# Kernel tuning notes

Measured on AMD Instinct MI355X. Metric: run time of the kernel, lower is better.

Reference implementation:

```python
import math
import jax, jax.numpy as jnp
import numpy as np

B, T, C = 2, 2048, 1024
NH, D = 16, 64


def setup_inputs() -> dict:
    key = jax.random.key(0)
    k1, k2, k3, k4 = jax.random.split(key, 4)
    x = jax.random.normal(k1, (B, T, C), dtype=jnp.float32)
    W_attn = jax.random.normal(k2, (3 * C, C), dtype=jnp.float32) * 0.02
    b_attn = jnp.zeros((3 * C,), dtype=jnp.float32)
    W_proj = jax.random.normal(k3, (C, C), dtype=jnp.float32) * 0.02
    b_proj = jnp.zeros((C,), dtype=jnp.float32)
    bV = jax.random.normal(k4, (NH, D), dtype=jnp.float32) * 0.05
    return {"x": x, "W_attn": W_attn, "b_attn": b_attn,
            "W_proj": W_proj, "b_proj": b_proj, "bV": bV}


def reference(x, W_attn, b_attn, W_proj, b_proj, bV):
    Bb, Tt, Cc = x.shape
    # fused qkv projection (torch Linear: x @ W.T + b)
    qkv = x @ W_attn.T + b_attn                     # [B,T,3C]
    q, k, v = jnp.split(qkv, 3, axis=2)
    q = q.reshape(Bb, Tt, NH, D).transpose(0, 2, 1, 3)  # [B,H,T,D]
    k = k.reshape(Bb, Tt, NH, D).transpose(0, 2, 1, 3)
    v = v.reshape(Bb, Tt, NH, D).transpose(0, 2, 1, 3)
    v = v + bV[None, :, None, :]                    # V-O symmetry-breaking bias
    scores = jnp.einsum('bhqd,bhkd->bhqk', q, k) / math.sqrt(D)
    causal = jnp.tril(jnp.ones((Tt, Tt), dtype=bool))
    scores = jnp.where(causal[None, None], scores, -jnp.inf)
    att = jax.nn.softmax(scores, axis=-1)           # [B,H,T,T]
    y = jnp.einsum('bhqk,bhkd->bhqd', att, v)
    y = y.transpose(0, 2, 1, 3).reshape(Bb, Tt, Cc)
    return y @ W_proj.T + b_proj
```

## Files before the change

kernel.cpp:

```cpp
#include <hip/hip_runtime.h>

#define DEVI __device__ __forceinline__

typedef __bf16 bf16x8 __attribute__((ext_vector_type(8)));
typedef float  f32x4  __attribute__((ext_vector_type(4)));

static DEVI unsigned short f2bf(float f) {
  unsigned u = __builtin_bit_cast(unsigned, f);
  u = u + 0x7fffu + ((u >> 16) & 1u);
  return (unsigned short)(u >> 16);
}
static DEVI unsigned short f2bf_trunc(float f) {
  return (unsigned short)(__builtin_bit_cast(unsigned, f) >> 16);
}

#define EXP2F(x) __builtin_amdgcn_exp2f(x)

typedef __attribute__((address_space(3))) void* lds_vp;
typedef const __attribute__((address_space(1))) void* glob_vp;
#define GL2LDS16(g, l) __builtin_amdgcn_global_load_lds((glob_vp)(g), (lds_vp)(l), 16, 0, 0)

__global__ void __launch_bounds__(256) conv_bf16(const float* __restrict__ in,
                                                 unsigned short* __restrict__ out, int n4) {
  int i = (int)blockIdx.x * 256 + (int)threadIdx.x;
  if (i >= n4) return;
  float4 v = reinterpret_cast<const float4*>(in)[i];
  ushort4 o;
  o.x = f2bf(v.x); o.y = f2bf(v.y); o.z = f2bf(v.z); o.w = f2bf(v.w);
  reinterpret_cast<ushort4*>(out)[i] = o;
}

#define GSTAGE(t_, bufi_) do {                                                    \
    const int kk_ = (t_)*64;                                                      \
    _Pragma("unroll")                                                             \
    for (int jq = 0; jq < 4; jq++) {                                              \
      const int row_ = w*32 + jq*8 + (l >> 3);                                    \
      GL2LDS16(A  + (size_t)(r0 + row_)*K + kk_ + scol, &sA[bufi_][(w*32 + jq*8)*64]); \
      GL2LDS16(Bm + (size_t)(c0 + row_)*K + kk_ + scol, &sB[bufi_][(w*32 + jq*8)*64]); \
    } } while (0)

template<int EPI>
__global__ void __launch_bounds__(256) gemm_bt(
    const unsigned short* __restrict__ A,
    const unsigned short* __restrict__ Bm,
    const float* __restrict__ bias,
    const float* __restrict__ bV,
    unsigned short* __restrict__ outQ,
    unsigned short* __restrict__ outK,
    unsigned short* __restrict__ outVT,
    float* __restrict__ outF)
{
  constexpr int K = 1024;
  constexpr int NSTEP = 16;
  __shared__ unsigned short sA[2][128*64];
  __shared__ unsigned short sB[2][128*64];
  const int tid = (int)threadIdx.x;
  const int w = tid >> 6;
  const int l = tid & 63;
  const int l15 = l & 15, lg = l >> 4;
  const int r0 = (int)blockIdx.y * 128;
  const int c0 = (int)blockIdx.x * 128;
  const int wr = (w >> 1) * 64, wc = (w & 1) * 64;
  const int scol = ((l & 7) ^ (l >> 3)) * 8;
  const int rdsw = (l & 7) * 8;

  f32x4 acc[4][4];
#pragma unroll
  for (int i = 0; i < 4; i++)
#pragma unroll
    for (int j = 0; j < 4; j++) acc[i][j] = (f32x4){0.f, 0.f, 0.f, 0.f};

  GSTAGE(0, 0);
  GSTAGE(1, 1);
  for (int t = 0; t < NSTEP; t++) {
    if (t < NSTEP-1) asm volatile("s_waitcnt vmcnt(8)" ::: "memory");
    else             asm volatile("s_waitcnt vmcnt(0)" ::: "memory");
    __builtin_amdgcn_s_barrier();
    const int bufi = t & 1;
    bf16x8 av[2][4], bv[2][4];
#pragma unroll
    for (int ks = 0; ks < 2; ks++) {
#pragma unroll
      for (int mi = 0; mi < 4; mi++)
        av[ks][mi] = *(const bf16x8*)&sA[bufi][(wr + mi*16 + l15)*64 + ((ks*32 + lg*8) ^ rdsw)];
#pragma unroll
      for (int ni = 0; ni < 4; ni++)
        bv[ks][ni] = *(const bf16x8*)&sB[bufi][(wc + ni*16 + l15)*64 + ((ks*32 + lg*8) ^ rdsw)];
    }
    asm volatile("s_waitcnt lgkmcnt(0)" ::: "memory");
    __builtin_amdgcn_s_barrier();
    if (t + 2 < NSTEP) GSTAGE(t + 2, bufi);
#pragma unroll
    for (int ks = 0; ks < 2; ks++)
#pragma unroll
      for (int mi = 0; mi < 4; mi++)
#pragma unroll
        for (int ni = 0; ni < 4; ni++)
          acc[mi][ni] = __builtin_amdgcn_mfma_f32_16x16x32_bf16(av[ks][mi], bv[ks][ni], acc[mi][ni], 0, 0, 0);
  }

#pragma unroll
  for (int mi = 0; mi < 4; mi++) {
    const int rbase = r0 + wr + mi*16 + lg*4;
#pragma unroll
    for (int ni = 0; ni < 4; ni++) {
      const int c = c0 + wc + ni*16 + l15;
      const float bsv = bias[c];
      if constexpr (EPI == 0) {
        const int which = c >> 10;
        const int cc = c & 1023;
        const int h = cc >> 6;
        const int d = cc & 63;
        const float bvv = (which == 2) ? bV[h*64 + d] : 0.f;
#pragma unroll
        for (int i = 0; i < 4; i++) {
          const int rr = rbase + i;
          const int b = rr >> 11;
          const int t = rr & 2047;
          const int bh = b*16 + h;
          const float v = acc[mi][ni][i] + bsv;
          if (which == 0)      outQ[((size_t)bh*2048 + t)*64 + d] = f2bf(v * 0.1803368801f);
          else if (which == 1) outK[((size_t)bh*2048 + t)*64 + d] = f2bf(v);
          else                 outVT[((size_t)bh*64 + d)*2048 + t] = f2bf(v + bvv);
        }
      } else {
#pragma unroll
        for (int i = 0; i < 4; i++)
          outF[(size_t)(rbase + i)*1024 + c] = acc[mi][ni][i] + bsv;
      }
    }
  }
}

#define ASTAGE(kt_, bufi_) do {                                                   \
    _Pragma("unroll")                                                             \
    for (int jq = 0; jq < 2; jq++) {                                              \
      const int chunk_ = w*2 + jq;                                                \
      GL2LDS16(Kh + (size_t)((kt_)*64 + chunk_*8 + (l >> 3))*64 + srcsw, &sK[bufi_][chunk_*512]); \
      GL2LDS16(Vh + (size_t)(chunk_*8 + (l >> 3))*2048 + (kt_)*64 + srcsw, &sV[bufi_][chunk_*512]); \
    } } while (0)

__global__ void __launch_bounds__(256) attn_fwd(
    const unsigned short* __restrict__ Q,
    const unsigned short* __restrict__ Kc,
    const unsigned short* __restrict__ VT,
    unsigned short* __restrict__ att)
{
  __shared__ unsigned short sK[2][64*64];
  __shared__ unsigned short sV[2][64*64];
  __shared__ unsigned short sP[4][16*64];

  const int tid = (int)threadIdx.x;
  const int w = tid >> 6, l = tid & 63;
  const int l15 = l & 15, lg = l >> 4;
  const int bh = (int)blockIdx.x;
  const int qt = (int)gridDim.y - 1 - (int)blockIdx.y;
  const int qw = qt * 64 + w * 16;

  const unsigned short* Qh = Q  + (size_t)bh * (2048*64);
  const unsigned short* Kh = Kc + (size_t)bh * (2048*64);
  const unsigned short* Vh = VT + (size_t)bh * (2048*64);

  bf16x8 qf[2];
#pragma unroll
  for (int ks = 0; ks < 2; ks++)
    qf[ks] = *(const bf16x8*)&Qh[(size_t)(qw + l15)*64 + ks*32 + lg*8];

  f32x4 o[4];
#pragma unroll
  for (int nd = 0; nd < 4; nd++) o[nd] = (f32x4){0.f, 0.f, 0.f, 0.f};
  float mrun[4], lpart[4];
#pragma unroll
  for (int i = 0; i < 4; i++) { mrun[i] = -1e30f; lpart[i] = 0.f; }

  const int srcsw = ((l & 7) ^ (l >> 3)) * 8;
  const int rdsw  = (l15 & 7) * 8;

  ASTAGE(0, 0);
  if (qt >= 1) ASTAGE(1, 1);
  for (int kt = 0; kt <= qt; kt++) {
    if (kt < qt) asm volatile("s_waitcnt vmcnt(4)" ::: "memory");
    else         asm volatile("s_waitcnt vmcnt(0)" ::: "memory");
    __builtin_amdgcn_s_barrier();
    const int bufi = kt & 1;
    {
      f32x4 s[4];
#pragma unroll
      for (int ni = 0; ni < 4; ni++) s[ni] = (f32x4){0.f, 0.f, 0.f, 0.f};
#pragma unroll
      for (int ks = 0; ks < 2; ks++) {
        bf16x8 kb[4];
#pragma unroll
        for (int ni = 0; ni < 4; ni++)
          kb[ni] = *(const bf16x8*)&sK[bufi][(ni*16 + l15)*64 + ((ks*32 + lg*8) ^ rdsw)];
        __builtin_amdgcn_s_setprio(1);
#pragma unroll
        for (int ni = 0; ni < 4; ni++)
          s[ni] = __builtin_amdgcn_mfma_f32_16x16x32_bf16(qf[ks], kb[ni], s[ni], 0, 0, 0);
        __builtin_amdgcn_s_setprio(0);
      }
      if (kt == qt) {
#pragma unroll
        for (int i = 0; i < 4; i++) {
          const int qq = qw + lg*4 + i;
#pragma unroll
          for (int ni = 0; ni < 4; ni++) {
            const int key = kt*64 + ni*16 + l15;
            if (key > qq) s[ni][i] = -1e30f;
          }
        }
      }
      unsigned short* pw = &sP[w][0];
#pragma unroll
      for (int i = 0; i < 4; i++) {
        float mx = fmaxf(fmaxf(s[0][i], s[1][i]), fmaxf(s[2][i], s[3][i]));
        mx = fmaxf(mx, __shfl_xor(mx, 1));
        mx = fmaxf(mx, __shfl_xor(mx, 2));
        mx = fmaxf(mx, __shfl_xor(mx, 4));
        mx = fmaxf(mx, __shfl_xor(mx, 8));
        if (mx > mrun[i]) {
          const float f = EXP2F(mrun[i] - mx);
          mrun[i] = mx;
          lpart[i] *= f;
#pragma unroll
          for (int nd = 0; nd < 4; nd++) o[nd][i] *= f;
        }
        const float mn = mrun[i];
        float ps = 0.f;
        const int row = lg*4 + i;
        const int psw = (row & 7) << 3;
#pragma unroll
        for (int ni = 0; ni < 4; ni++) {
          const float p = EXP2F(s[ni][i] - mn);
          ps += p;
          pw[row*64 + ((ni*16 + l15) ^ psw)] = f2bf_trunc(p);
        }
        lpart[i] += ps;
      }
#pragma unroll
      for (int ks = 0; ks < 2; ks++) {
        bf16x8 pf, vb[4];
        pf = *(const bf16x8*)&pw[l15*64 + ((ks*32 + lg*8) ^ rdsw)];
#pragma unroll
        for (int nd = 0; nd < 4; nd++)
          vb[nd] = *(const bf16x8*)&sV[bufi][(nd*16 + l15)*64 + ((ks*32 + lg*8) ^ rdsw)];
        __builtin_amdgcn_s_setprio(1);
#pragma unroll
        for (int nd = 0; nd < 4; nd++)
          o[nd] = __builtin_amdgcn_mfma_f32_16x16x32_bf16(pf, vb[nd], o[nd], 0, 0, 0);
        __builtin_amdgcn_s_setprio(0);
      }
    }
    asm volatile("s_waitcnt lgkmcnt(0)" ::: "memory");
    __builtin_amdgcn_s_barrier();
    if (kt + 2 <= qt) ASTAGE(kt + 2, bufi);
  }

  const int b = bh >> 4, h = bh & 15;
#pragma unroll
  for (int i = 0; i < 4; i++) {
    float lp = lpart[i];
    lp += __shfl_xor(lp, 1);
    lp += __shfl_xor(lp, 2);
    lp += __shfl_xor(lp, 4);
    lp += __shfl_xor(lp, 8);
    const float rinv = 1.0f / lp;
    const int qq = qw + lg*4 + i;
#pragma unroll
    for (int nd = 0; nd < 4; nd++) {
      const int d = nd*16 + l15;
      att[((size_t)(b*2048 + qq))*1024 + h*64 + d] = f2bf(o[nd][i] * rinv);
    }
  }
}

extern "C" void kernel_launch(void* const* d_in, const int* in_sizes, int n_in,
                              void* d_out, int out_size, void* d_ws, size_t ws_size,
                              hipStream_t stream) {
  const float* x      = (const float*)d_in[0];
  const float* W_attn = (const float*)d_in[1];
  const float* b_attn = (const float*)d_in[2];
  const float* W_proj = (const float*)d_in[3];
  const float* b_proj = (const float*)d_in[4];
  const float* bV     = (const float*)d_in[5];
  float* out = (float*)d_out;
  char* ws = (char*)d_ws;

  unsigned short* xb   = (unsigned short*)(ws);
  unsigned short* wab  = (unsigned short*)(ws + (8u  << 20));
  unsigned short* wpb  = (unsigned short*)(ws + (14u << 20));
  unsigned short* qb   = (unsigned short*)(ws + (16u << 20));
  unsigned short* kb   = (unsigned short*)(ws + (24u << 20));
  unsigned short* vtb  = (unsigned short*)(ws + (32u << 20));
  unsigned short* attb = (unsigned short*)(ws + (40u << 20));

  conv_bf16<<<4096, 256, 0, stream>>>(x,      xb,  1048576);
  conv_bf16<<<3072, 256, 0, stream>>>(W_attn, wab,  786432);
  conv_bf16<<<1024, 256, 0, stream>>>(W_proj, wpb,  262144);

  gemm_bt<0><<<dim3(24, 32), 256, 0, stream>>>(xb, wab, b_attn, bV, qb, kb, vtb, nullptr);
  attn_fwd<<<dim3(32, 32), 256, 0, stream>>>(qb, kb, vtb, attb);
  gemm_bt<1><<<dim3(8, 32), 256, 0, stream>>>(attb, wpb, b_proj, nullptr, nullptr, nullptr, nullptr, out);
}
```

Measured before the change: 145.6 us.

## Load K/V tiles per-wave directly from global, dropping LDS staging and barriers

Removes the shared-memory double-buffered K/V staging (global_load_lds plus block barriers) from the attention kernel. Each wave now loads its K and V^T fragments straight from global memory into registers and runs its own causal loop bound (qw>>6), so waves skip tiles they do not need and never synchronise with each other. The cost is four-fold redundant global/L2 traffic across the waves of a block, with no software prefetch to hide load latency.

```diff
diff --git a/kernel.cpp b/kernel.cpp
--- a/kernel.cpp
+++ b/kernel.cpp
@@ -132,22 +132,12 @@
   }
 }
 
-#define ASTAGE(kt_, bufi_) do {                                                   \
-    _Pragma("unroll")                                                             \
-    for (int jq = 0; jq < 2; jq++) {                                              \
-      const int chunk_ = w*2 + jq;                                                \
-      GL2LDS16(Kh + (size_t)((kt_)*64 + chunk_*8 + (l >> 3))*64 + srcsw, &sK[bufi_][chunk_*512]); \
-      GL2LDS16(Vh + (size_t)(chunk_*8 + (l >> 3))*2048 + (kt_)*64 + srcsw, &sV[bufi_][chunk_*512]); \
-    } } while (0)
-
 __global__ void __launch_bounds__(256) attn_fwd(
     const unsigned short* __restrict__ Q,
     const unsigned short* __restrict__ Kc,
     const unsigned short* __restrict__ VT,
     unsigned short* __restrict__ att)
 {
-  __shared__ unsigned short sK[2][64*64];
-  __shared__ unsigned short sV[2][64*64];
   __shared__ unsigned short sP[4][16*64];
 
   const int tid = (int)threadIdx.x;
@@ -173,87 +163,81 @@
 #pragma unroll
   for (int i = 0; i < 4; i++) { mrun[i] = -1e30f; lpart[i] = 0.f; }
 
-  const int srcsw = ((l & 7) ^ (l >> 3)) * 8;
-  const int rdsw  = (l15 & 7) * 8;
-
-  ASTAGE(0, 0);
-  if (qt >= 1) ASTAGE(1, 1);
-  for (int kt = 0; kt <= qt; kt++) {
-    if (kt < qt) asm volatile("s_waitcnt vmcnt(4)" ::: "memory");
-    else         asm volatile("s_waitcnt vmcnt(0)" ::: "memory");
-    __builtin_amdgcn_s_barrier();
-    const int bufi = kt & 1;
-    {
-      f32x4 s[4];
-#pragma unroll
-      for (int ni = 0; ni < 4; ni++) s[ni] = (f32x4){0.f, 0.f, 0.f, 0.f};
-#pragma unroll
-      for (int ks = 0; ks < 2; ks++) {
-        bf16x8 kb[4];
-#pragma unroll
-        for (int ni = 0; ni < 4; ni++)
-          kb[ni] = *(const bf16x8*)&sK[bufi][(ni*16 + l15)*64 + ((ks*32 + lg*8) ^ rdsw)];
-        __builtin_amdgcn_s_setprio(1);
-#pragma unroll
-        for (int ni = 0; ni < 4; ni++)
-          s[ni] = __builtin_amdgcn_mfma_f32_16x16x32_bf16(qf[ks], kb[ni], s[ni], 0, 0, 0);
-        __builtin_amdgcn_s_setprio(0);
-      }
-      if (kt == qt) {
-#pragma unroll
-        for (int i = 0; i < 4; i++) {
-          const int qq = qw + lg*4 + i;
-#pragma unroll
-          for (int ni = 0; ni < 4; ni++) {
-            const int key = kt*64 + ni*16 + l15;
-            if (key > qq) s[ni][i] = -1e30f;
-          }
+  const int rdsw = (l15 & 7) * 8;
+
+  const int ktmax = qw >> 6;
+  for (int kt = 0; kt <= ktmax; kt++) {
+    const unsigned short* Kt = Kh + (size_t)kt * (64*64);
+    f32x4 s[4];
+#pragma unroll
+    for (int ni = 0; ni < 4; ni++) s[ni] = (f32x4){0.f, 0.f, 0.f, 0.f};
+    bf16x8 kb[2][4];
+#pragma unroll
+    for (int ks = 0; ks < 2; ks++)
+#pragma unroll
+      for (int ni = 0; ni < 4; ni++)
+        kb[ks][ni] = *(const bf16x8*)&Kt[(ni*16 + l15)*64 + ks*32 + lg*8];
+#pragma unroll
+    for (int ks = 0; ks < 2; ks++) {
+      __builtin_amdgcn_s_setprio(1);
+#pragma unroll
+      for (int ni = 0; ni < 4; ni++)
+        s[ni] = __builtin_amdgcn_mfma_f32_16x16x32_bf16(qf[ks], kb[ks][ni], s[ni], 0, 0, 0);
+      __builtin_amdgcn_s_setprio(0);
+    }
+    bf16x8 vb[2][4];
+#pragma unroll
+    for (int ks = 0; ks < 2; ks++)
+#pragma unroll
+      for (int nd = 0; nd < 4; nd++)
+        vb[ks][nd] = *(const bf16x8*)&Vh[(size_t)(nd*16 + l15)*2048 + kt*64 + ks*32 + lg*8];
+    if (kt == ktmax) {
+#pragma unroll
+      for (int i = 0; i < 4; i++) {
+        const int qq = qw + lg*4 + i;
+#pragma unroll
+        for (int ni = 0; ni < 4; ni++) {
+          const int key = kt*64 + ni*16 + l15;
+          if (key > qq) s[ni][i] = -1e30f;
         }
       }
-      unsigned short* pw = &sP[w][0];
-#pragma unroll
-      for (int i = 0; i < 4; i++) {
-        float mx = fmaxf(fmaxf(s[0][i], s[1][i]), fmaxf(s[2][i], s[3][i]));
-        mx = fmaxf(mx, __shfl_xor(mx, 1));
-        mx = fmaxf(mx, __shfl_xor(mx, 2));
-        mx = fmaxf(mx, __shfl_xor(mx, 4));
-        mx = fmaxf(mx, __shfl_xor(mx, 8));
-        if (mx > mrun[i]) {
-          const float f = EXP2F(mrun[i] - mx);
-          mrun[i] = mx;
-          lpart[i] *= f;
-#pragma unroll
-          for (int nd = 0; nd < 4; nd++) o[nd][i] *= f;
-        }
-        const float mn = mrun[i];
-        float ps = 0.f;
-        const int row = lg*4 + i;
-        const int psw = (row & 7) << 3;
-#pragma unroll
-        for (int ni = 0; ni < 4; ni++) {
-          const float p = EXP2F(s[ni][i] - mn);
-          ps += p;
-          pw[row*64 + ((ni*16 + l15) ^ psw)] = f2bf_trunc(p);
-        }
-        lpart[i] += ps;
-      }
-#pragma unroll
-      for (int ks = 0; ks < 2; ks++) {
-        bf16x8 pf, vb[4];
-        pf = *(const bf16x8*)&pw[l15*64 + ((ks*32 + lg*8) ^ rdsw)];
-#pragma unroll
-        for (int nd = 0; nd < 4; nd++)
-          vb[nd] = *(const bf16x8*)&sV[bufi][(nd*16 + l15)*64 + ((ks*32 + lg*8) ^ rdsw)];
-        __builtin_amdgcn_s_setprio(1);
-#pragma unroll
-        for (int nd = 0; nd < 4; nd++)
-          o[nd] = __builtin_amdgcn_mfma_f32_16x16x32_bf16(pf, vb[nd], o[nd], 0, 0, 0);
-        __builtin_amdgcn_s_setprio(0);
-      }
-    }
-    asm volatile("s_waitcnt lgkmcnt(0)" ::: "memory");
-    __builtin_amdgcn_s_barrier();
-    if (kt + 2 <= qt) ASTAGE(kt + 2, bufi);
+    }
+    unsigned short* pw = &sP[w][0];
+#pragma unroll
+    for (int i = 0; i < 4; i++) {
+      float mx = fmaxf(fmaxf(s[0][i], s[1][i]), fmaxf(s[2][i], s[3][i]));
+      mx = fmaxf(mx, __shfl_xor(mx, 1));
+      mx = fmaxf(mx, __shfl_xor(mx, 2));
+      mx = fmaxf(mx, __shfl_xor(mx, 4));
+      mx = fmaxf(mx, __shfl_xor(mx, 8));
+      if (mx > mrun[i]) {
+        const float f = EXP2F(mrun[i] - mx);
+        mrun[i] = mx;
+        lpart[i] *= f;
+#pragma unroll
+        for (int nd = 0; nd < 4; nd++) o[nd][i] *= f;
+      }
+      const float mn = mrun[i];
+      float ps = 0.f;
+      const int row = lg*4 + i;
+      const int psw = (row & 7) << 3;
+#pragma unroll
+      for (int ni = 0; ni < 4; ni++) {
+        const float p = EXP2F(s[ni][i] - mn);
+        ps += p;
+        pw[row*64 + ((ni*16 + l15) ^ psw)] = f2bf_trunc(p);
+      }
+      lpart[i] += ps;
+    }
+#pragma unroll
+    for (int ks = 0; ks < 2; ks++) {
+      bf16x8 pf = *(const bf16x8*)&pw[l15*64 + ((ks*32 + lg*8) ^ rdsw)];
+      __builtin_amdgcn_s_setprio(1);
+#pragma unroll
+      for (int nd = 0; nd < 4; nd++)
+        o[nd] = __builtin_amdgcn_mfma_f32_16x16x32_bf16(pf, vb[ks][nd], o[nd], 0, 0, 0);
+      __builtin_amdgcn_s_setprio(0);
+    }
   }
 
   const int b = bh >> 4, h = bh & 15;
```

Measured after the change: 205.9 us. +41.4%, slower.
